# Kernel tuning notes

Measured on AMD Instinct MI355X. Metric: run time of the kernel, lower is better.

The kernel has to match this reference:

```python
import jax, jax.numpy as jnp
import numpy as np

D_MODEL = 1024
N_HEADS = 16
HEAD_DIM = D_MODEL // N_HEADS
ALPHA = 1.5
SEQ, BATCH = 4096, 8


def reduced_sparsemax(z, alpha):
    # projection of z/alpha onto the simplex along the last axis
    zs = z / alpha
    z_sorted = -jnp.sort(-zs, axis=-1)          # descending sort
    z_cumsum = jnp.cumsum(z_sorted, axis=-1)
    d = zs.shape[-1]
    r = jnp.arange(1, d + 1, dtype=zs.dtype)
    support = (z_sorted - (z_cumsum - 1.0) / r) > 0
    k = jnp.sum(support, axis=-1, keepdims=True)
    k_safe = jnp.clip(k, 1, None)
    tau_sum = jnp.take_along_axis(z_cumsum, k_safe - 1, axis=-1)
    tau = (tau_sum - 1.0) / k_safe.astype(zs.dtype)
    return jnp.clip(zs - tau, 0.0, None)


def setup_inputs() -> dict:
    key = jax.random.key(0)
    ks = jax.random.split(key, 11)
    s = 0.02
    return {
        "query": jax.random.normal(ks[0], (SEQ, BATCH, D_MODEL), jnp.float32),
        "key":   jax.random.normal(ks[1], (SEQ, BATCH, D_MODEL), jnp.float32),
        "value": jax.random.normal(ks[2], (SEQ, BATCH, D_MODEL), jnp.float32),
        "Wq": jax.random.normal(ks[3], (D_MODEL, D_MODEL), jnp.float32) * s,
        "bq": jnp.zeros((D_MODEL,), jnp.float32),
        "Wk": jax.random.normal(ks[4], (D_MODEL, D_MODEL), jnp.float32) * s,
        "bk": jnp.zeros((D_MODEL,), jnp.float32),
        "Wv": jax.random.normal(ks[5], (D_MODEL, D_MODEL), jnp.float32) * s,
        "bv": jnp.zeros((D_MODEL,), jnp.float32),
        "Wo": jax.random.normal(ks[6], (D_MODEL, D_MODEL), jnp.float32) * s,
        "bo": jnp.zeros((D_MODEL,), jnp.float32),
    }


def reference(query, key, value, Wq, bq, Wk, bk, Wv, bv, Wo, bo):
    A, B, D = query.shape  # (seq, batch, d_model) per the torch code's indexing
    H, hd = N_HEADS, HEAD_DIM
    Q = query @ Wq.T + bq
    K = key @ Wk.T + bk
    V = value @ Wv.T + bv
    # view(A, B, H, hd).transpose(0, 1) -> (B, A, H, hd)
    Q = jnp.swapaxes(Q.reshape(A, B, H, hd), 0, 1)
    K = jnp.swapaxes(K.reshape(A, B, H, hd), 0, 1)
    V = jnp.swapaxes(V.reshape(A, B, H, hd), 0, 1)
    # NOTE: faithful to the original code, attention is across HEADS:
    # scores shape (B, A, H, H)
    scores = jnp.einsum('bahd,bagd->bahg', Q, K) / jnp.sqrt(
        jnp.asarray(hd, jnp.float32))
    attn = reduced_sparsemax(scores, ALPHA)
    attn_out = jnp.einsum('bahg,bagd->bahd', attn, V)  # (B, A, H, hd)
    # transpose(1,2).view(B, -1, D): (B, H, A, hd) flattened to (B, A, D)
    attn_out = jnp.swapaxes(attn_out, 1, 2).reshape(B, -1, D)
    out = attn_out @ Wo.T + bo           # (B, A, D)
    return jnp.swapaxes(out, 0, 1)       # (A, B, D)
```

## Files before the change

kernel.cpp:

```cpp
#include <hip/hip_runtime.h>
#include <hip/hip_bf16.h>
#include <stdint.h>

typedef __bf16 bf16_t;
typedef __bf16 bf16x4 __attribute__((ext_vector_type(4)));
typedef __bf16 bf16x8 __attribute__((ext_vector_type(8)));
typedef float  f32x4  __attribute__((ext_vector_type(4)));

#define AS_G __attribute__((address_space(1)))
#define AS_L __attribute__((address_space(3)))

__global__ void cast_f32_bf16(const float* __restrict__ src, bf16_t* __restrict__ dst) {
    int i = blockIdx.x * 256 + threadIdx.x;
    float4 v = ((const float4*)src)[i];
    bf16x4 o;
    o.x = (bf16_t)v.x; o.y = (bf16_t)v.y; o.z = (bf16_t)v.z; o.w = (bf16_t)v.w;
    ((bf16x4*)dst)[i] = o;
}

template<int OUT_BF16>
__global__ void gemm_bt_kernel(const bf16_t* __restrict__ A,
                               const bf16_t* __restrict__ Bt,
                               const float* __restrict__ bias,
                               void* __restrict__ Cout,
                               int M, int N, int K) {
    __shared__ bf16_t As[128 * 32];
    __shared__ bf16_t Bs[128 * 32];
    const int tid  = threadIdx.x;
    const int wave = tid >> 6, lane = tid & 63;
    const int quad = lane >> 4, r16 = lane & 15;
    const int wm = (wave >> 1) * 64, wn = (wave & 1) * 64;
    const int m0 = blockIdx.y * 128, n0 = blockIdx.x * 128;

    const int sr = (wave << 5) + (lane >> 2);
    const int ce = (lane & 3) << 3;
    const bf16_t* ga = A  + (size_t)(m0 + sr) * K + ce;
    const bf16_t* gb = Bt + (size_t)(n0 + sr) * K + ce;
    bf16_t* la = &As[sr * 32 + ce];
    bf16_t* lb = &Bs[sr * 32 + ce];

    f32x4 acc[4][4] = {};

    for (int k0 = 0; k0 < K; k0 += 32) {
        __builtin_amdgcn_global_load_lds((AS_G void*)(ga + k0),              (AS_L void*)la,             16, 0, 0);
        __builtin_amdgcn_global_load_lds((AS_G void*)(ga + k0 + 16 * (size_t)K), (AS_L void*)(la + 16 * 32), 16, 0, 0);
        __builtin_amdgcn_global_load_lds((AS_G void*)(gb + k0),              (AS_L void*)lb,             16, 0, 0);
        __builtin_amdgcn_global_load_lds((AS_G void*)(gb + k0 + 16 * (size_t)K), (AS_L void*)(lb + 16 * 32), 16, 0, 0);
        __syncthreads();

        bf16x8 aF[4], bF[4];
#pragma unroll
        for (int t = 0; t < 4; ++t) {
            aF[t] = *(const bf16x8*)&As[(wm + t * 16 + r16) * 32 + quad * 8];
            bF[t] = *(const bf16x8*)&Bs[(wn + t * 16 + r16) * 32 + quad * 8];
        }
#pragma unroll
        for (int tm = 0; tm < 4; ++tm)
#pragma unroll
            for (int tn = 0; tn < 4; ++tn)
                acc[tm][tn] = __builtin_amdgcn_mfma_f32_16x16x32_bf16(aF[tm], bF[tn], acc[tm][tn], 0, 0, 0);
        __syncthreads();
    }

    float bv[4];
#pragma unroll
    for (int tn = 0; tn < 4; ++tn) bv[tn] = bias[n0 + wn + tn * 16 + r16];

#pragma unroll
    for (int tm = 0; tm < 4; ++tm) {
#pragma unroll
        for (int r = 0; r < 4; ++r) {
            const int m = m0 + wm + tm * 16 + quad * 4 + r;
#pragma unroll
            for (int tn = 0; tn < 4; ++tn) {
                const int n = n0 + wn + tn * 16 + r16;
                const float v = acc[tm][tn][r] + bv[tn];
                if (OUT_BF16) ((bf16_t*)Cout)[(size_t)m * N + n] = (bf16_t)v;
                else          ((float*)Cout)[(size_t)m * N + n]  = v;
            }
        }
    }
}

__global__ void attn_kernel(const bf16_t* __restrict__ Q, const bf16_t* __restrict__ K,
                            const bf16_t* __restrict__ V, bf16_t* __restrict__ M2) {
    __shared__ float zs_s[4][16][17];
    __shared__ float tau_s[4][16];
    const int wave = threadIdx.x >> 6, lane = threadIdx.x & 63;
    const int quad = lane >> 4, g16 = lane & 15;
    const int p = blockIdx.x * 4 + wave;
    const int a = p >> 3, b = p & 7;
    const bf16_t* q = Q + (size_t)p * 1024;
    const bf16_t* k = K + (size_t)p * 1024;
    const bf16_t* v = V + (size_t)p * 1024;

    bf16x8 qa0 = *(const bf16x8*)(q + g16 * 64 + quad * 8);
    bf16x8 qa1 = *(const bf16x8*)(q + g16 * 64 + 32 + quad * 8);
    bf16x8 ka0 = *(const bf16x8*)(k + g16 * 64 + quad * 8);
    bf16x8 ka1 = *(const bf16x8*)(k + g16 * 64 + 32 + quad * 8);
    f32x4 sc = {0.f, 0.f, 0.f, 0.f};
    sc = __builtin_amdgcn_mfma_f32_16x16x32_bf16(qa0, ka0, sc, 0, 0, 0);
    sc = __builtin_amdgcn_mfma_f32_16x16x32_bf16(qa1, ka1, sc, 0, 0, 0);

    const float inv = 1.0f / 12.0f;
#pragma unroll
    for (int r = 0; r < 4; ++r) zs_s[wave][quad * 4 + r][g16] = sc[r] * inv;
    __syncthreads();

    if (lane < 16) {
        float z[16];
#pragma unroll
        for (int j = 0; j < 16; ++j) z[j] = zs_s[wave][lane][j];
#pragma unroll
        for (int kk = 2; kk <= 16; kk <<= 1) {
#pragma unroll
            for (int j = kk >> 1; j > 0; j >>= 1) {
#pragma unroll
                for (int i = 0; i < 16; ++i) {
                    int ixj = i ^ j;
                    if (ixj > i) {
                        bool desc = ((i & kk) == 0);
                        float zi = z[i], zj = z[ixj];
                        bool sw = desc ? (zi < zj) : (zi > zj);
                        z[i]   = sw ? zj : zi;
                        z[ixj] = sw ? zi : zj;
                    }
                }
            }
        }
        float cum = 0.f, csel = 0.f;
        int ksel = 1;
#pragma unroll
        for (int j = 0; j < 16; ++j) {
            cum += z[j];
            bool sup = z[j] * (float)(j + 1) > (cum - 1.0f);
            ksel = sup ? (j + 1) : ksel;
            csel = sup ? cum : csel;
        }
        tau_s[wave][lane] = (csel - 1.0f) / (float)ksel;
    }
    __syncthreads();

#pragma unroll
    for (int r = 0; r < 4; ++r) {
        float av = sc[r] * inv - tau_s[wave][quad * 4 + r];
        zs_s[wave][quad * 4 + r][g16] = av > 0.f ? av : 0.f;
    }
    __syncthreads();

    bf16x8 aP;
#pragma unroll
    for (int j = 0; j < 8; ++j) {
        float f = (quad < 2) ? zs_s[wave][g16][quad * 8 + j] : 0.f;
        aP[j] = (bf16_t)f;
    }
#pragma unroll
    for (int c = 0; c < 4; ++c) {
        bf16x8 bV;
#pragma unroll
        for (int j = 0; j < 8; ++j) {
            int g = quad * 8 + j;
            bV[j] = (quad < 2) ? v[g * 64 + c * 16 + g16] : (bf16_t)0.f;
        }
        f32x4 oc = {0.f, 0.f, 0.f, 0.f};
        oc = __builtin_amdgcn_mfma_f32_16x16x32_bf16(aP, bV, oc, 0, 0, 0);
#pragma unroll
        for (int r = 0; r < 4; ++r) {
            int h = quad * 4 + r;
            int e = c * 16 + g16;
            int rr = (h << 8) + (a >> 4);
            int c2 = ((a & 15) << 6) + e;
            M2[((size_t)(rr * 8 + b)) * 1024 + c2] = (bf16_t)oc[r];
        }
    }
}

extern "C" void kernel_launch(void* const* d_in, const int* in_sizes, int n_in,
                              void* d_out, int out_size, void* d_ws, size_t ws_size,
                              hipStream_t stream) {
    (void)in_sizes; (void)n_in; (void)out_size; (void)ws_size;
    const float* query = (const float*)d_in[0];
    const float* key   = (const float*)d_in[1];
    const float* value = (const float*)d_in[2];
    const float* Wq = (const float*)d_in[3];
    const float* bq = (const float*)d_in[4];
    const float* Wk = (const float*)d_in[5];
    const float* bk = (const float*)d_in[6];
    const float* Wv = (const float*)d_in[7];
    const float* bv = (const float*)d_in[8];
    const float* Wo = (const float*)d_in[9];
    const float* bo = (const float*)d_in[10];

    const int M = 32768, D = 1024;
    const size_t MD = (size_t)M * D;

    uint8_t* ws = (uint8_t*)d_ws;
    bf16_t* abuf = (bf16_t*)ws;
    bf16_t* Qb   = (bf16_t*)(ws + MD * 2);
    bf16_t* Kb   = Qb + MD;
    bf16_t* Vb   = Kb + MD;
    bf16_t* M2   = Vb + MD;
    bf16_t* Wqb  = M2 + MD;
    bf16_t* Wkb  = Wqb + (size_t)D * D;
    bf16_t* Wvb  = Wkb + (size_t)D * D;
    bf16_t* Wob  = Wvb + (size_t)D * D;

    const int wBlocks = D * D / 1024;
    const int aBlocks = (int)(MD / 1024);
    cast_f32_bf16<<<wBlocks, 256, 0, stream>>>(Wq, Wqb);
    cast_f32_bf16<<<wBlocks, 256, 0, stream>>>(Wk, Wkb);
    cast_f32_bf16<<<wBlocks, 256, 0, stream>>>(Wv, Wvb);
    cast_f32_bf16<<<wBlocks, 256, 0, stream>>>(Wo, Wob);

    dim3 gg(D / 128, M / 128);

    cast_f32_bf16<<<aBlocks, 256, 0, stream>>>(query, abuf);
    gemm_bt_kernel<1><<<gg, 256, 0, stream>>>(abuf, Wqb, bq, Qb, M, D, D);
    cast_f32_bf16<<<aBlocks, 256, 0, stream>>>(key, abuf);
    gemm_bt_kernel<1><<<gg, 256, 0, stream>>>(abuf, Wkb, bk, Kb, M, D, D);
    cast_f32_bf16<<<aBlocks, 256, 0, stream>>>(value, abuf);
    gemm_bt_kernel<1><<<gg, 256, 0, stream>>>(abuf, Wvb, bv, Vb, M, D, D);

    attn_kernel<<<M / 4, 256, 0, stream>>>(Qb, Kb, Vb, M2);

    gemm_bt_kernel<0><<<gg, 256, 0, stream>>>(M2, Wob, bo, (float*)d_out, M, D, D);
}
```

Before: 875.6 us.

## Fuse activation casts into QKV GEMM, batch launches, swizzle LDS, stage V transpose

```diff
diff --git a/kernel.cpp b/kernel.cpp
--- a/kernel.cpp
+++ b/kernel.cpp
@@ -10,56 +10,125 @@
 #define AS_G __attribute__((address_space(1)))
 #define AS_L __attribute__((address_space(3)))
 
-__global__ void cast_f32_bf16(const float* __restrict__ src, bf16_t* __restrict__ dst) {
-    int i = blockIdx.x * 256 + threadIdx.x;
+struct CastArgs { const float* s0; const float* s1; const float* s2; const float* s3; bf16_t* dst; };
+
+__global__ void cast_weights(CastArgs c) {
+    const int w = blockIdx.x >> 10;
+    const float* src = (w == 0) ? c.s0 : (w == 1) ? c.s1 : (w == 2) ? c.s2 : c.s3;
+    const int i = (blockIdx.x & 1023) * 256 + threadIdx.x;
     float4 v = ((const float4*)src)[i];
     bf16x4 o;
     o.x = (bf16_t)v.x; o.y = (bf16_t)v.y; o.z = (bf16_t)v.z; o.w = (bf16_t)v.w;
-    ((bf16x4*)dst)[i] = o;
-}
-
-template<int OUT_BF16>
-__global__ void gemm_bt_kernel(const bf16_t* __restrict__ A,
-                               const bf16_t* __restrict__ Bt,
-                               const float* __restrict__ bias,
-                               void* __restrict__ Cout,
-                               int M, int N, int K) {
-    __shared__ bf16_t As[128 * 32];
-    __shared__ bf16_t Bs[128 * 32];
+    ((bf16x4*)(c.dst + ((size_t)w << 20)))[i] = o;
+}
+
+template<int A_F32, int OUT_BF16>
+__device__ __forceinline__ void gemm_core(const void* __restrict__ Av,
+                                          const bf16_t* __restrict__ Bt,
+                                          const float* __restrict__ bias,
+                                          void* __restrict__ Cout,
+                                          int M, int N, int K, int m0, int n0,
+                                          void* AsRaw, bf16_t* __restrict__ Bs) {
     const int tid  = threadIdx.x;
     const int wave = tid >> 6, lane = tid & 63;
     const int quad = lane >> 4, r16 = lane & 15;
     const int wm = (wave >> 1) * 64, wn = (wave & 1) * 64;
-    const int m0 = blockIdx.y * 128, n0 = blockIdx.x * 128;
-
-    const int sr = (wave << 5) + (lane >> 2);
-    const int ce = (lane & 3) << 3;
-    const bf16_t* ga = A  + (size_t)(m0 + sr) * K + ce;
-    const bf16_t* gb = Bt + (size_t)(n0 + sr) * K + ce;
-    bf16_t* la = &As[sr * 32 + ce];
-    bf16_t* lb = &Bs[sr * 32 + ce];
+
+    const int brow = lane >> 2;
+    const int cb   = (lane & 3) ^ ((lane >> 3) & 3);
+    const bf16_t* gb = Bt + (size_t)(n0 + (wave << 5) + brow) * K + cb * 8;
+    bf16_t* lb = Bs + ((wave << 5) + brow) * 32 + (lane & 3) * 8;
+
+    const int fb = (r16 >> 1) & 3;
+    int boff[4];
+#pragma unroll
+    for (int t = 0; t < 4; ++t)
+        boff[t] = (wn + t * 16 + r16) * 32 + ((quad ^ fb) << 3);
 
     f32x4 acc[4][4] = {};
 
-    for (int k0 = 0; k0 < K; k0 += 32) {
-        __builtin_amdgcn_global_load_lds((AS_G void*)(ga + k0),              (AS_L void*)la,             16, 0, 0);
-        __builtin_amdgcn_global_load_lds((AS_G void*)(ga + k0 + 16 * (size_t)K), (AS_L void*)(la + 16 * 32), 16, 0, 0);
-        __builtin_amdgcn_global_load_lds((AS_G void*)(gb + k0),              (AS_L void*)lb,             16, 0, 0);
-        __builtin_amdgcn_global_load_lds((AS_G void*)(gb + k0 + 16 * (size_t)K), (AS_L void*)(lb + 16 * 32), 16, 0, 0);
-        __syncthreads();
-
-        bf16x8 aF[4], bF[4];
+    if (A_F32) {
+        const float* A = (const float*)Av;
+        float* Asf = (float*)AsRaw;
+        const int arow = lane >> 3;
+        const int ca   = (lane & 7) ^ arow;
+        const float* ga = A + (size_t)(m0 + (wave << 5) + arow) * K + ca * 4;
+        float* la = Asf + ((wave << 5) + arow) * 32 + (lane & 7) * 4;
+
+        const int fa = r16 & 7;
+        int aoff0[4], aoff1[4];
 #pragma unroll
         for (int t = 0; t < 4; ++t) {
-            aF[t] = *(const bf16x8*)&As[(wm + t * 16 + r16) * 32 + quad * 8];
-            bF[t] = *(const bf16x8*)&Bs[(wn + t * 16 + r16) * 32 + quad * 8];
-        }
-#pragma unroll
-        for (int tm = 0; tm < 4; ++tm)
-#pragma unroll
-            for (int tn = 0; tn < 4; ++tn)
-                acc[tm][tn] = __builtin_amdgcn_mfma_f32_16x16x32_bf16(aF[tm], bF[tn], acc[tm][tn], 0, 0, 0);
-        __syncthreads();
+            const int rowA = (wm + t * 16 + r16) * 32;
+            aoff0[t] = rowA + (((2 * quad    ) ^ fa) << 2);
+            aoff1[t] = rowA + (((2 * quad + 1) ^ fa) << 2);
+        }
+
+        for (int k0 = 0; k0 < K; k0 += 32) {
+#pragma unroll
+            for (int t = 0; t < 4; ++t)
+                __builtin_amdgcn_global_load_lds((const AS_G void*)(ga + (size_t)t * 8 * K + k0),
+                                                 (AS_L void*)(la + t * 256), 16, 0, 0);
+#pragma unroll
+            for (int t = 0; t < 2; ++t)
+                __builtin_amdgcn_global_load_lds((const AS_G void*)(gb + (size_t)t * 16 * K + k0),
+                                                 (AS_L void*)(lb + t * 512), 16, 0, 0);
+            __syncthreads();
+
+            bf16x8 aF[4], bF[4];
+#pragma unroll
+            for (int t = 0; t < 4; ++t) {
+                f32x4 a0 = *(const f32x4*)&Asf[aoff0[t]];
+                f32x4 a1 = *(const f32x4*)&Asf[aoff1[t]];
+                bf16x8 af;
+#pragma unroll
+                for (int j = 0; j < 4; ++j) { af[j] = (bf16_t)a0[j]; af[4 + j] = (bf16_t)a1[j]; }
+                aF[t] = af;
+                bF[t] = *(const bf16x8*)&Bs[boff[t]];
+            }
+#pragma unroll
+            for (int tm = 0; tm < 4; ++tm)
+#pragma unroll
+                for (int tn = 0; tn < 4; ++tn)
+                    acc[tm][tn] = __builtin_amdgcn_mfma_f32_16x16x32_bf16(aF[tm], bF[tn], acc[tm][tn], 0, 0, 0);
+            __syncthreads();
+        }
+    } else {
+        const bf16_t* A = (const bf16_t*)Av;
+        bf16_t* As = (bf16_t*)AsRaw;
+        const int arow = lane >> 2;
+        const int caA  = (lane & 3) ^ ((lane >> 3) & 3);
+        const bf16_t* ga = A + (size_t)(m0 + (wave << 5) + arow) * K + caA * 8;
+        bf16_t* la = As + ((wave << 5) + arow) * 32 + (lane & 3) * 8;
+
+        int aoff[4];
+#pragma unroll
+        for (int t = 0; t < 4; ++t)
+            aoff[t] = (wm + t * 16 + r16) * 32 + ((quad ^ fb) << 3);
+
+        for (int k0 = 0; k0 < K; k0 += 32) {
+#pragma unroll
+            for (int t = 0; t < 2; ++t) {
+                __builtin_amdgcn_global_load_lds((const AS_G void*)(ga + (size_t)t * 16 * K + k0),
+                                                 (AS_L void*)(la + t * 512), 16, 0, 0);
+                __builtin_amdgcn_global_load_lds((const AS_G void*)(gb + (size_t)t * 16 * K + k0),
+                                                 (AS_L void*)(lb + t * 512), 16, 0, 0);
+            }
+            __syncthreads();
+
+            bf16x8 aF[4], bF[4];
+#pragma unroll
+            for (int t = 0; t < 4; ++t) {
+                aF[t] = *(const bf16x8*)&As[aoff[t]];
+                bF[t] = *(const bf16x8*)&Bs[boff[t]];
+            }
+#pragma unroll
+            for (int tm = 0; tm < 4; ++tm)
+#pragma unroll
+                for (int tn = 0; tn < 4; ++tn)
+                    acc[tm][tn] = __builtin_amdgcn_mfma_f32_16x16x32_bf16(aF[tm], bF[tn], acc[tm][tn], 0, 0, 0);
+            __syncthreads();
+        }
     }
 
     float bv[4];
@@ -82,10 +151,38 @@
     }
 }
 
+struct QkvArgs {
+    const float* A0; const float* A1; const float* A2;
+    const bf16_t* Bt;
+    const float* b0; const float* b1; const float* b2;
+    bf16_t* C;
+};
+
+__global__ __launch_bounds__(256) void gemm_qkv(QkvArgs q, int M, int N, int K) {
+    __shared__ float  Asf[128 * 32];
+    __shared__ bf16_t Bs[128 * 32];
+    const int z = blockIdx.z;
+    const float* A    = (z == 0) ? q.A0 : (z == 1) ? q.A1 : q.A2;
+    const float* bias = (z == 0) ? q.b0 : (z == 1) ? q.b1 : q.b2;
+    gemm_core<1, 1>(A, q.Bt + (size_t)z * N * K, bias, q.C + (size_t)z * M * N,
+                    M, N, K, blockIdx.y * 128, blockIdx.x * 128, Asf, Bs);
+}
+
+__global__ __launch_bounds__(256) void gemm_out(const bf16_t* __restrict__ A,
+                                                const bf16_t* __restrict__ Bt,
+                                                const float* __restrict__ bias,
+                                                float* __restrict__ C,
+                                                int M, int N, int K) {
+    __shared__ bf16_t As[128 * 32];
+    __shared__ bf16_t Bs[128 * 32];
+    gemm_core<0, 0>(A, Bt, bias, C, M, N, K, blockIdx.y * 128, blockIdx.x * 128, As, Bs);
+}
+
 __global__ void attn_kernel(const bf16_t* __restrict__ Q, const bf16_t* __restrict__ K,
                             const bf16_t* __restrict__ V, bf16_t* __restrict__ M2) {
-    __shared__ float zs_s[4][16][17];
-    __shared__ float tau_s[4][16];
+    __shared__ bf16_t vt[4][2048];
+    __shared__ float  zs_s[4][16][17];
+    __shared__ float  tau_s[4][16];
     const int wave = threadIdx.x >> 6, lane = threadIdx.x & 63;
     const int quad = lane >> 4, g16 = lane & 15;
     const int p = blockIdx.x * 4 + wave;
@@ -98,6 +195,20 @@
     bf16x8 qa1 = *(const bf16x8*)(q + g16 * 64 + 32 + quad * 8);
     bf16x8 ka0 = *(const bf16x8*)(k + g16 * 64 + quad * 8);
     bf16x8 ka1 = *(const bf16x8*)(k + g16 * 64 + 32 + quad * 8);
+    bf16x8 v0  = *(const bf16x8*)(v + lane * 16);
+    bf16x8 v1  = *(const bf16x8*)(v + lane * 16 + 8);
+
+    {
+        bf16_t* vtw = vt[wave];
+        const int g = lane >> 2, gh = g >> 3, gl = g & 7;
+        const int eb = (lane & 3) * 16;
+#pragma unroll
+        for (int j = 0; j < 16; ++j) {
+            const int e = eb + j;
+            vtw[e * 32 + ((gh ^ ((e >> 1) & 3)) << 3) + gl] = (j < 8) ? v0[j] : v1[j - 8];
+        }
+    }
+
     f32x4 sc = {0.f, 0.f, 0.f, 0.f};
     sc = __builtin_amdgcn_mfma_f32_16x16x32_bf16(qa0, ka0, sc, 0, 0, 0);
     sc = __builtin_amdgcn_mfma_f32_16x16x32_bf16(qa1, ka1, sc, 0, 0, 0);
@@ -150,28 +261,44 @@
 
     bf16x8 aP;
 #pragma unroll
-    for (int j = 0; j < 8; ++j) {
-        float f = (quad < 2) ? zs_s[wave][g16][quad * 8 + j] : 0.f;
-        aP[j] = (bf16_t)f;
-    }
+    for (int j = 0; j < 8; ++j)
+        aP[j] = (quad < 2) ? (bf16_t)zs_s[wave][g16][quad * 8 + j] : (bf16_t)0.f;
+
+    const bf16_t* vtw = vt[wave];
+    const int fv = (g16 >> 1) & 3;
+    f32x4 oc[4];
 #pragma unroll
     for (int c = 0; c < 4; ++c) {
         bf16x8 bV;
-#pragma unroll
-        for (int j = 0; j < 8; ++j) {
-            int g = quad * 8 + j;
-            bV[j] = (quad < 2) ? v[g * 64 + c * 16 + g16] : (bf16_t)0.f;
-        }
-        f32x4 oc = {0.f, 0.f, 0.f, 0.f};
-        oc = __builtin_amdgcn_mfma_f32_16x16x32_bf16(aP, bV, oc, 0, 0, 0);
-#pragma unroll
-        for (int r = 0; r < 4; ++r) {
-            int h = quad * 4 + r;
-            int e = c * 16 + g16;
-            int rr = (h << 8) + (a >> 4);
-            int c2 = ((a & 15) << 6) + e;
-            M2[((size_t)(rr * 8 + b)) * 1024 + c2] = (bf16_t)oc[r];
-        }
+        if (quad < 2) {
+            bV = *(const bf16x8*)&vtw[(c * 16 + g16) * 32 + ((quad ^ fv) << 3)];
+        } else {
+#pragma unroll
+            for (int j = 0; j < 8; ++j) bV[j] = (bf16_t)0.f;
+        }
+        f32x4 z4 = {0.f, 0.f, 0.f, 0.f};
+        oc[c] = __builtin_amdgcn_mfma_f32_16x16x32_bf16(aP, bV, z4, 0, 0, 0);
+    }
+    __syncthreads();
+
+    {
+        bf16_t* ob = vt[wave];
+#pragma unroll
+        for (int c = 0; c < 4; ++c)
+#pragma unroll
+            for (int r = 0; r < 4; ++r)
+                ob[(quad * 4 + r) * 72 + c * 16 + g16] = (bf16_t)oc[c][r];
+    }
+    __syncthreads();
+    {
+        const bf16_t* ob = vt[wave];
+        const int hh = lane >> 2, e0 = (lane & 3) * 16;
+        bf16x8 o0 = *(const bf16x8*)&ob[hh * 72 + e0];
+        bf16x8 o1 = *(const bf16x8*)&ob[hh * 72 + e0 + 8];
+        const size_t m2row = (size_t)(hh * 256 + (a >> 4)) * 8 + b;
+        bf16_t* dst = M2 + m2row * 1024 + ((a & 15) << 6) + e0;
+        *(bf16x8*)dst = o0;
+        *(bf16x8*)(dst + 8) = o1;
     }
 }
 
@@ -194,34 +321,20 @@
     const int M = 32768, D = 1024;
     const size_t MD = (size_t)M * D;
 
-    uint8_t* ws = (uint8_t*)d_ws;
-    bf16_t* abuf = (bf16_t*)ws;
-    bf16_t* Qb   = (bf16_t*)(ws + MD * 2);
-    bf16_t* Kb   = Qb + MD;
-    bf16_t* Vb   = Kb + MD;
-    bf16_t* M2   = Vb + MD;
-    bf16_t* Wqb  = M2 + MD;
-    bf16_t* Wkb  = Wqb + (size_t)D * D;
-    bf16_t* Wvb  = Wkb + (size_t)D * D;
-    bf16_t* Wob  = Wvb + (size_t)D * D;
-
-    const int wBlocks = D * D / 1024;
-    const int aBlocks = (int)(MD / 1024);
-    cast_f32_bf16<<<wBlocks, 256, 0, stream>>>(Wq, Wqb);
-    cast_f32_bf16<<<wBlocks, 256, 0, stream>>>(Wk, Wkb);
-    cast_f32_bf16<<<wBlocks, 256, 0, stream>>>(Wv, Wvb);
-    cast_f32_bf16<<<wBlocks, 256, 0, stream>>>(Wo, Wob);
-
-    dim3 gg(D / 128, M / 128);
-
-    cast_f32_bf16<<<aBlocks, 256, 0, stream>>>(query, abuf);
-    gemm_bt_kernel<1><<<gg, 256, 0, stream>>>(abuf, Wqb, bq, Qb, M, D, D);
-    cast_f32_bf16<<<aBlocks, 256, 0, stream>>>(key, abuf);
-    gemm_bt_kernel<1><<<gg, 256, 0, stream>>>(abuf, Wkb, bk, Kb, M, D, D);
-    cast_f32_bf16<<<aBlocks, 256, 0, stream>>>(value, abuf);
-    gemm_bt_kernel<1><<<gg, 256, 0, stream>>>(abuf, Wvb, bv, Vb, M, D, D);
+    bf16_t* Qb = (bf16_t*)d_ws;
+    bf16_t* Kb = Qb + MD;
+    bf16_t* Vb = Kb + MD;
+    bf16_t* M2 = Vb + MD;
+    bf16_t* Wb = M2 + MD;
+
+    CastArgs ca = {Wq, Wk, Wv, Wo, Wb};
+    cast_weights<<<4096, 256, 0, stream>>>(ca);
+
+    QkvArgs qa = {query, key, value, Wb, bq, bk, bv, Qb};
+    gemm_qkv<<<dim3(D / 128, M / 128, 3), 256, 0, stream>>>(qa, M, D, D);
 
     attn_kernel<<<M / 4, 256, 0, stream>>>(Qb, Kb, Vb, M2);
 
-    gemm_bt_kernel<0><<<gg, 256, 0, stream>>>(M2, Wob, bo, (float*)d_out, M, D, D);
-}
+    gemm_out<<<dim3(D / 128, M / 128), 256, 0, stream>>>(M2, Wb + 3 * (size_t)D * D, bo,
+                                                         (float*)d_out, M, D, D);
+}
```

Result: slower. 911.2 us (+4.1%).
